# Optimization experiments

Hardware: AMD Instinct MI355X
Metric: run time of the kernel (lower is better)

## Reference

```python
import jax, jax.numpy as jnp
import numpy as np

# --- module hyperparameters (from init_kwargs / defaults) ---
CUTOFF = 4.5
NUM_RADIAL = 8
L_MAX = 2
RHO_U_DEGREE = 3
MAG_REF = 2.2
EPS = 1e-8
U_REF = max(MAG_REF * MAG_REF, EPS)

_centers_np = np.linspace(0.0, CUTOFF, NUM_RADIAL).astype(np.float32)
_spacing = float(_centers_np[1] - _centers_np[0]) if NUM_RADIAL > 1 else CUTOFF
BETA = 1.0 / max(_spacing * _spacing, EPS)
CENTERS = jnp.asarray(_centers_np)

N_ATOMS = 20000
N_NEIGH = 32


def cutoff_fn(r):
    x = jnp.clip(jnp.pi * r / CUTOFF, 0.0, jnp.pi)
    y = 0.5 * (jnp.cos(x) + 1.0)
    return y * (r < CUTOFF).astype(r.dtype)


def radial_basis(r):
    # r: [...], returns [..., NUM_RADIAL]
    diff = r[..., None] - CENTERS
    radial = jnp.exp(-BETA * diff * diff)
    return radial * cutoff_fn(r)[..., None]


def legendre_basis(x):
    # x: [...], returns [..., L_MAX + 1] via standard recurrence
    x = jnp.clip(x, -1.0, 1.0)
    polys = [jnp.ones_like(x)]
    if L_MAX >= 1:
        polys.append(x)
    for l in range(1, L_MAX):
        p_lp1 = ((2 * l + 1) * x * polys[-1] - l * polys[-2]) / (l + 1)
        polys.append(p_lp1)
    return jnp.stack(polys, axis=-1)


def setup_inputs() -> dict:
    key = jax.random.key(0)
    k1, k2, k3 = jax.random.split(key, 3)
    # positions in a small box so random-neighbor distances land inside the cutoff
    pos = jax.random.uniform(k1, (N_ATOMS, 3), dtype=jnp.float32) * 3.0
    mag = jax.random.normal(k2, (N_ATOMS, 3), dtype=jnp.float32)
    neigh_idx = jax.random.randint(k3, (N_ATOMS, N_NEIGH), 0, N_ATOMS)
    return {"pos": pos, "mag": mag, "neigh_idx": neigh_idx}


def reference(pos, mag, neigh_idx):
    N, K = neigh_idx.shape
    # gather neighbor geometry: [N, K, 3]
    vec = pos[neigh_idx] - pos[:, None, :]
    dist = jnp.sqrt(jnp.sum(vec * vec, axis=-1) + EPS)  # [N, K]
    f = radial_basis(dist)  # [N, K, R]

    # --- radial geometric channel ---
    rho_r = jnp.sum(f, axis=1)  # [N, R]

    # --- onsite longitudinal channel (power basis) ---
    u = jnp.sum(mag * mag, axis=-1)  # [N]
    u_norm = u / U_REF
    rho_u = jnp.stack([u_norm ** p for p in range(1, RHO_U_DEGREE + 1)], axis=-1)  # [N, 3]

    # --- neighbor magnetic channels ---
    mag_j = mag[neigh_idx]        # [N, K, 3]
    u_j = u_norm[neigh_idx]       # [N, K]
    rho_uj = jnp.einsum('nk,nkr->nr', u_j, f)                      # [N, R]
    s = jnp.einsum('nd,nkd->nk', mag, mag_j) / U_REF               # m_i . m_j / u_ref
    rho_s = jnp.einsum('nk,nkr->nr', s, f)                         # [N, R]

    # --- angular (triplet) channels, unique neighbor pairs j < k ---
    cos = jnp.einsum('njd,nkd->njk', vec, vec) / (dist[:, :, None] * dist[:, None, :] + EPS)
    P = legendre_basis(cos)  # [N, K, K, L+1]
    mask = jnp.triu(jnp.ones((K, K), dtype=f.dtype), k=1)  # j < k
    Pm = P * mask[None, :, :, None]

    A_rr = jnp.einsum('njkl,nja,nkb->nabl', Pm, f, f).reshape(N, -1)

    w_jk = jnp.einsum('njd,nkd->njk', mag_j, mag_j) / U_REF  # m_j . m_k / u_ref
    A_jk = jnp.einsum('njkl,nja,nkb->nabl', Pm * w_jk[..., None], f, f).reshape(N, -1)

    w_imm = s[:, :, None] * s[:, None, :]  # (m_i.m_j)(m_i.m_k) / u_ref^2
    A_imm = jnp.einsum('njkl,nja,nkb->nabl', Pm * w_imm[..., None], f, f).reshape(N, -1)

    # descriptor layout: rho_u | rho_r | A_rr | rho_uj | rho_s | A_jk | A_imm
    return jnp.concatenate([rho_u, rho_r, A_rr, rho_uj, rho_s, A_jk, A_imm], axis=-1)
```

## Files before the change

### kernel.cpp

```cpp
#include <hip/hip_runtime.h>

#define K 32
#define DESC 603

typedef _Float16 h8  __attribute__((ext_vector_type(8)));
typedef _Float16 h4v __attribute__((ext_vector_type(4)));
typedef __fp16   fp16x2 __attribute__((ext_vector_type(2)));
typedef float    f32x4 __attribute__((ext_vector_type(4)));

#define WAVE_LDS_FENCE()  __asm__ volatile("s_waitcnt lgkmcnt(0)" ::: "memory")
#define COMPILER_BARRIER() __asm__ volatile("" ::: "memory")

#define SFT   0
#define GTB   256
#define UHX   2304
#define UHY   2336
#define UHZ   2368
#define MJX   2400
#define MJY   2432
#define MJZ   2464
#define SSK   2496
#define SUK   2528
#define JPK   2560

__device__ __forceinline__ h8 h8splat(float x) {
    _Float16 h = (_Float16)x;
    h8 r = {h,h,h,h,h,h,h,h};
    return r;
}
__device__ __forceinline__ h8 bc(_Float16 h) {
    h8 r = {h,h,h,h,h,h,h,h};
    return r;
}
__device__ __forceinline__ h4v pk4(const f32x4& a) {
    fp16x2 lo = __builtin_amdgcn_cvt_pkrtz(a[0], a[1]);
    fp16x2 hi = __builtin_amdgcn_cvt_pkrtz(a[2], a[3]);
    h4v r;
    r[0] = (_Float16)lo[0]; r[1] = (_Float16)lo[1];
    r[2] = (_Float16)hi[0]; r[3] = (_Float16)hi[1];
    return r;
}

__global__ __launch_bounds__(256, 6)
void desc_kernel(const float* __restrict__ pos, const float* __restrict__ mag,
                 const int* __restrict__ nidx, float* __restrict__ out, int natoms)
{
    __shared__ __align__(16) _Float16 ldsbuf[4][2816];
    const int w = threadIdx.x >> 6;
    const int l = threadIdx.x & 63;
    int atom0 = blockIdx.x * 4 + w;
    const bool act = atom0 < natoms;
    if (!act) atom0 = natoms - 1;
    const int atom = __builtin_amdgcn_readfirstlane(atom0);
    _Float16* W = &ldsbuf[w][0];

    const int col  = l & 15;
    const int quad = l >> 4;
    const int k0   = quad * 8;

    const float CUTOFF  = 4.5f;
    const float SPACING = CUTOFF / 7.0f;
    const float BETA    = 1.0f / (SPACING * SPACING);
    const float INV_U   = 1.0f / 4.84f;
    const float INV_MAG = 1.0f / 2.2f;
    const float PI_F    = 3.14159265358979f;

    const float pix = pos[3*atom+0], piy = pos[3*atom+1], piz = pos[3*atom+2];
    const float mix = mag[3*atom+0], miy = mag[3*atom+1], miz = mag[3*atom+2];

    const int k = l & 31;
    const int n = nidx[atom*K + k];
    const float* src = (l < K) ? (pos + 3*n) : (mag + 3*n);
    const float v0 = src[0], v1 = src[1], v2 = src[2];

    if (l < K) {
        const float vx = v0 - pix, vy = v1 - piy, vz = v2 - piz;
        const float d  = sqrtf(vx*vx + vy*vy + vz*vz + 1e-8f);
        const float rd = 1.0f / d;
        const _Float16 hx = (_Float16)(vx*rd), hy = (_Float16)(vy*rd), hz = (_Float16)(vz*rd);
        W[UHX+k] = hx; W[UHY+k] = hy; W[UHZ+k] = hz;
        h4v jp = {hx, hy, hz, (_Float16)0.0f};
        *(h4v*)&W[JPK + k*8] = jp;
        float cut = 0.0f;
        if (d < CUTOFF) cut = 0.5f * (__cosf(PI_F * d / CUTOFF) + 1.0f);
        #pragma unroll
        for (int r = 0; r < 8; ++r) {
            const float diff = d - (float)r * SPACING;
            W[SFT + r*32 + k] = (_Float16)(__expf(-BETA * diff * diff) * cut);
        }
    } else {
        const float mx = v0*INV_MAG, my = v1*INV_MAG, mz = v2*INV_MAG;
        const float ss = (mix*v0 + miy*v1 + miz*v2) * INV_U;
        const float su = (v0*v0 + v1*v1 + v2*v2) * INV_U;
        const _Float16 hmx = (_Float16)mx, hmy = (_Float16)my, hmz = (_Float16)mz;
        const _Float16 hss = (_Float16)ss, hsu = (_Float16)su;
        W[MJX+k] = hmx; W[MJY+k] = hmy; W[MJZ+k] = hmz;
        W[SSK+k] = hss; W[SUK+k] = hsu;
        h4v jp = {hmx, hmy, hmz, hss};
        *(h4v*)&W[JPK + k*8 + 4] = jp;
    }
    if (l == 32 && act) {
        const float un = (mix*mix + miy*miy + miz*miz) * INV_U;
        out[atom*DESC+0] = un; out[atom*DESC+1] = un*un; out[atom*DESC+2] = un*un*un;
    }
    WAVE_LDS_FENCE();

    const h8 Bf   = *(const h8*)&W[SFT + (col&7)*32 + k0];
    const h8 uhx8 = *(const h8*)&W[UHX + k0];
    const h8 uhy8 = *(const h8*)&W[UHY + k0];
    const h8 uhz8 = *(const h8*)&W[UHZ + k0];
    const h8 mjx8 = *(const h8*)&W[MJX + k0];
    const h8 mjy8 = *(const h8*)&W[MJY + k0];
    const h8 mjz8 = *(const h8*)&W[MJZ + k0];
    const h8 ssk8 = *(const h8*)&W[SSK + k0];
    const h8 suk8 = *(const h8*)&W[SUK + k0];
    COMPILER_BARRIER();

    {
        h8 Ar = h8splat(0.0f);
        if      (col == 0) Ar = h8splat(1.0f);
        else if (col == 1) Ar = suk8;
        else if (col == 2) Ar = ssk8;
        f32x4 d = __builtin_amdgcn_mfma_f32_16x16x32_f16(Ar, Bf, (f32x4){0,0,0,0}, 0,0,0);
        if (act && quad == 0 && col < 8) {
            out[atom*DESC + 3   + col] = d[0];
            out[atom*DESC + 203 + col] = d[1];
            out[atom*DESC + 211 + col] = d[2];
        }
    }

    #pragma unroll
    for (int t = 0; t < 2; ++t) {
        const int j  = t*16 + col;
        const h8 jp  = *(const h8*)&W[JPK + j*8];
        h8 c = uhx8*bc(jp[0]) + uhy8*bc(jp[1]) + uhz8*bc(jp[2]);
        c = __builtin_elementwise_min(h8splat(1.0f),
            __builtin_elementwise_max(h8splat(-1.0f), c));
        const h8 P1 = c;
        const h8 P2 = c * c * h8splat(1.5f) - h8splat(0.5f);
        h8 wv  = mjx8*bc(jp[4]) + mjy8*bc(jp[5]) + mjz8*bc(jp[6]);
        h8 wiv = ssk8*bc(jp[7]);
        h8 mk;
        #pragma unroll
        for (int e = 0; e < 8; ++e)
            mk[e] = (_Float16)((k0 + e > j) ? 1.0f : 0.0f);

        const int tcol = t*16 + quad*4;
        const f32x4 z4 = {0,0,0,0};
        #pragma unroll
        for (int ch = 0; ch < 3; ++ch) {
            const h8 Bv = (ch == 0) ? mk : (ch == 1) ? wv*mk : wiv*mk;
            f32x4 a0 = __builtin_amdgcn_mfma_f32_16x16x32_f16(Bv,    Bf, z4, 0,0,0);
            f32x4 a1 = __builtin_amdgcn_mfma_f32_16x16x32_f16(Bv*P1, Bf, z4, 0,0,0);
            f32x4 a2 = __builtin_amdgcn_mfma_f32_16x16x32_f16(Bv*P2, Bf, z4, 0,0,0);
            if (col < 8) {
                const int row = ch*24 + col*3;
                *(h4v*)&W[GTB + (row+0)*32 + tcol] = pk4(a0);
                *(h4v*)&W[GTB + (row+1)*32 + tcol] = pk4(a1);
                *(h4v*)&W[GTB + (row+2)*32 + tcol] = pk4(a2);
            }
        }
    }
    WAVE_LDS_FENCE();

    #pragma unroll
    for (int nt = 0; nt < 5; ++nt) {
        const int n = nt*16 + col;
        const h8 Bg = *(const h8*)&W[GTB + n*32 + k0];
        const f32x4 d = __builtin_amdgcn_mfma_f32_16x16x32_f16(Bf, Bg, (f32x4){0,0,0,0}, 0,0,0);
        if (act && quad < 2 && n < 72) {
            const int ch  = n / 24;
            const int off = n - ch*24;
            const int cb  = (ch == 0) ? 11 : ((ch == 1) ? 219 : 411);
            const int base = atom*DESC + cb + off + quad*96;
            #pragma unroll
            for (int reg = 0; reg < 4; ++reg)
                out[base + reg*24] = d[reg];
        }
    }
}

extern "C" void kernel_launch(void* const* d_in, const int* in_sizes, int n_in,
                              void* d_out, int out_size, void* d_ws, size_t ws_size,
                              hipStream_t stream) {
    const float* pos  = (const float*)d_in[0];
    const float* mag  = (const float*)d_in[1];
    const int*   nidx = (const int*)d_in[2];
    float* out = (float*)d_out;
    const int n_atoms = in_sizes[2] / K;
    const int blocks = (n_atoms + 3) / 4;
    desc_kernel<<<blocks, 256, 0, stream>>>(pos, mag, nidx, out, n_atoms);
}
```

Baseline: 90.25 us.

## Process two atoms per wave and overlap the geometry and Gram buffers in LDS

Each wave now handles two atoms instead of one, using 128-thread blocks that still cover four atoms, so the gather, MFMA and store phases of two independent atoms can interleave. The per-atom LDS scratch is shrunk by placing the Gram-tile buffer over the radial-basis and direction arrays, which are already held in registers by the time they are overwritten. The aim is more instruction-level parallelism and less LDS use per atom. The cost is higher register pressure and a lower launch-bounds occupancy hint.

```diff
diff --git a/kernel.cpp b/kernel.cpp
--- a/kernel.cpp
+++ b/kernel.cpp
@@ -11,17 +11,17 @@
 #define WAVE_LDS_FENCE()  __asm__ volatile("s_waitcnt lgkmcnt(0)" ::: "memory")
 #define COMPILER_BARRIER() __asm__ volatile("" ::: "memory")
 
+#define GTB   0
 #define SFT   0
-#define GTB   256
-#define UHX   2304
-#define UHY   2336
-#define UHZ   2368
-#define MJX   2400
-#define MJY   2432
-#define MJZ   2464
-#define SSK   2496
-#define SUK   2528
-#define JPK   2560
+#define UHX   2048
+#define UHY   2080
+#define UHZ   2112
+#define MJX   2144
+#define MJY   2176
+#define MJZ   2208
+#define SSK   2240
+#define SUK   2272
+#define JPK   2304
 
 __device__ __forceinline__ h8 h8splat(float x) {
     _Float16 h = (_Float16)x;
@@ -41,19 +41,13 @@
     return r;
 }
 
-__global__ __launch_bounds__(256, 6)
+__global__ __launch_bounds__(128, 4)
 void desc_kernel(const float* __restrict__ pos, const float* __restrict__ mag,
                  const int* __restrict__ nidx, float* __restrict__ out, int natoms)
 {
-    __shared__ __align__(16) _Float16 ldsbuf[4][2816];
+    __shared__ __align__(16) _Float16 ldsbuf[4][2560];
     const int w = threadIdx.x >> 6;
     const int l = threadIdx.x & 63;
-    int atom0 = blockIdx.x * 4 + w;
-    const bool act = atom0 < natoms;
-    if (!act) atom0 = natoms - 1;
-    const int atom = __builtin_amdgcn_readfirstlane(atom0);
-    _Float16* W = &ldsbuf[w][0];
-
     const int col  = l & 15;
     const int quad = l >> 4;
     const int k0   = quad * 8;
@@ -65,117 +59,150 @@
     const float INV_MAG = 1.0f / 2.2f;
     const float PI_F    = 3.14159265358979f;
 
-    const float pix = pos[3*atom+0], piy = pos[3*atom+1], piz = pos[3*atom+2];
-    const float mix = mag[3*atom+0], miy = mag[3*atom+1], miz = mag[3*atom+2];
-
-    const int k = l & 31;
-    const int n = nidx[atom*K + k];
-    const float* src = (l < K) ? (pos + 3*n) : (mag + 3*n);
-    const float v0 = src[0], v1 = src[1], v2 = src[2];
-
-    if (l < K) {
-        const float vx = v0 - pix, vy = v1 - piy, vz = v2 - piz;
-        const float d  = sqrtf(vx*vx + vy*vy + vz*vz + 1e-8f);
-        const float rd = 1.0f / d;
-        const _Float16 hx = (_Float16)(vx*rd), hy = (_Float16)(vy*rd), hz = (_Float16)(vz*rd);
-        W[UHX+k] = hx; W[UHY+k] = hy; W[UHZ+k] = hz;
-        h4v jp = {hx, hy, hz, (_Float16)0.0f};
-        *(h4v*)&W[JPK + k*8] = jp;
-        float cut = 0.0f;
-        if (d < CUTOFF) cut = 0.5f * (__cosf(PI_F * d / CUTOFF) + 1.0f);
+    int       atomv[2];
+    bool      actv[2];
+    _Float16* Wv[2];
+    h8        Bfv[2];
+
+    #pragma unroll
+    for (int u = 0; u < 2; ++u) {
+        int a0 = blockIdx.x * 4 + w * 2 + u;
+        actv[u] = a0 < natoms;
+        if (!actv[u]) a0 = natoms - 1;
+        atomv[u] = __builtin_amdgcn_readfirstlane(a0);
+        Wv[u] = &ldsbuf[w * 2 + u][0];
+    }
+
+    #pragma unroll
+    for (int u = 0; u < 2; ++u) {
+        const int atom = atomv[u];
+        _Float16* W = Wv[u];
+        const float pix = pos[3*atom+0], piy = pos[3*atom+1], piz = pos[3*atom+2];
+        const float mix = mag[3*atom+0], miy = mag[3*atom+1], miz = mag[3*atom+2];
+
+        const int k = l & 31;
+        const int n = nidx[atom*K + k];
+        const float* src = (l < K) ? (pos + 3*n) : (mag + 3*n);
+        const float v0 = src[0], v1 = src[1], v2 = src[2];
+
+        if (l < K) {
+            const float vx = v0 - pix, vy = v1 - piy, vz = v2 - piz;
+            const float d  = sqrtf(vx*vx + vy*vy + vz*vz + 1e-8f);
+            const float rd = 1.0f / d;
+            const _Float16 hx = (_Float16)(vx*rd), hy = (_Float16)(vy*rd), hz = (_Float16)(vz*rd);
+            W[UHX+k] = hx; W[UHY+k] = hy; W[UHZ+k] = hz;
+            h4v jp = {hx, hy, hz, (_Float16)0.0f};
+            *(h4v*)&W[JPK + k*8] = jp;
+            float cut = 0.0f;
+            if (d < CUTOFF) cut = 0.5f * (__cosf(PI_F * d / CUTOFF) + 1.0f);
+            #pragma unroll
+            for (int r = 0; r < 8; ++r) {
+                const float diff = d - (float)r * SPACING;
+                W[SFT + r*32 + k] = (_Float16)(__expf(-BETA * diff * diff) * cut);
+            }
+        } else {
+            const float mx = v0*INV_MAG, my = v1*INV_MAG, mz = v2*INV_MAG;
+            const float ss = (mix*v0 + miy*v1 + miz*v2) * INV_U;
+            const float su = (v0*v0 + v1*v1 + v2*v2) * INV_U;
+            const _Float16 hmx = (_Float16)mx, hmy = (_Float16)my, hmz = (_Float16)mz;
+            W[MJX+k] = hmx; W[MJY+k] = hmy; W[MJZ+k] = hmz;
+            W[SSK+k] = (_Float16)ss; W[SUK+k] = (_Float16)su;
+            h4v jp = {hmx, hmy, hmz, (_Float16)ss};
+            *(h4v*)&W[JPK + k*8 + 4] = jp;
+        }
+        if (l == 32 && actv[u]) {
+            const float un = (mix*mix + miy*miy + miz*miz) * INV_U;
+            out[atom*DESC+0] = un; out[atom*DESC+1] = un*un; out[atom*DESC+2] = un*un*un;
+        }
+    }
+    WAVE_LDS_FENCE();
+
+    #pragma unroll
+    for (int u = 0; u < 2; ++u) {
+        const int atom = atomv[u];
+        const bool act = actv[u];
+        _Float16* W = Wv[u];
+
+        const h8 Bf   = *(const h8*)&W[SFT + (col&7)*32 + k0];
+        const h8 uhx8 = *(const h8*)&W[UHX + k0];
+        const h8 uhy8 = *(const h8*)&W[UHY + k0];
+        const h8 uhz8 = *(const h8*)&W[UHZ + k0];
+        const h8 mjx8 = *(const h8*)&W[MJX + k0];
+        const h8 mjy8 = *(const h8*)&W[MJY + k0];
+        const h8 mjz8 = *(const h8*)&W[MJZ + k0];
+        const h8 ssk8 = *(const h8*)&W[SSK + k0];
+        const h8 suk8 = *(const h8*)&W[SUK + k0];
+        Bfv[u] = Bf;
+        COMPILER_BARRIER();
+
+        {
+            h8 Ar = h8splat(0.0f);
+            if      (col == 0) Ar = h8splat(1.0f);
+            else if (col == 1) Ar = suk8;
+            else if (col == 2) Ar = ssk8;
+            f32x4 d = __builtin_amdgcn_mfma_f32_16x16x32_f16(Ar, Bf, (f32x4){0,0,0,0}, 0,0,0);
+            if (act && quad == 0 && col < 8) {
+                out[atom*DESC + 3   + col] = d[0];
+                out[atom*DESC + 203 + col] = d[1];
+                out[atom*DESC + 211 + col] = d[2];
+            }
+        }
+
         #pragma unroll
-        for (int r = 0; r < 8; ++r) {
-            const float diff = d - (float)r * SPACING;
-            W[SFT + r*32 + k] = (_Float16)(__expf(-BETA * diff * diff) * cut);
-        }
-    } else {
-        const float mx = v0*INV_MAG, my = v1*INV_MAG, mz = v2*INV_MAG;
-        const float ss = (mix*v0 + miy*v1 + miz*v2) * INV_U;
-        const float su = (v0*v0 + v1*v1 + v2*v2) * INV_U;
-        const _Float16 hmx = (_Float16)mx, hmy = (_Float16)my, hmz = (_Float16)mz;
-        const _Float16 hss = (_Float16)ss, hsu = (_Float16)su;
-        W[MJX+k] = hmx; W[MJY+k] = hmy; W[MJZ+k] = hmz;
-        W[SSK+k] = hss; W[SUK+k] = hsu;
-        h4v jp = {hmx, hmy, hmz, hss};
-        *(h4v*)&W[JPK + k*8 + 4] = jp;
-    }
-    if (l == 32 && act) {
-        const float un = (mix*mix + miy*miy + miz*miz) * INV_U;
-        out[atom*DESC+0] = un; out[atom*DESC+1] = un*un; out[atom*DESC+2] = un*un*un;
+        for (int t = 0; t < 2; ++t) {
+            const int j  = t*16 + col;
+            const h8 jp  = *(const h8*)&W[JPK + j*8];
+            h8 c = uhx8*bc(jp[0]) + uhy8*bc(jp[1]) + uhz8*bc(jp[2]);
+            c = __builtin_elementwise_min(h8splat(1.0f),
+                __builtin_elementwise_max(h8splat(-1.0f), c));
+            const h8 P1 = c;
+            const h8 P2 = c * c * h8splat(1.5f) - h8splat(0.5f);
+            h8 wv  = mjx8*bc(jp[4]) + mjy8*bc(jp[5]) + mjz8*bc(jp[6]);
+            h8 wiv = ssk8*bc(jp[7]);
+            h8 mk;
+            #pragma unroll
+            for (int e = 0; e < 8; ++e)
+                mk[e] = (_Float16)((k0 + e > j) ? 1.0f : 0.0f);
+
+            const int tcol = t*16 + quad*4;
+            const f32x4 z4 = {0,0,0,0};
+            #pragma unroll
+            for (int ch = 0; ch < 3; ++ch) {
+                const h8 Bv = (ch == 0) ? mk : (ch == 1) ? wv*mk : wiv*mk;
+                f32x4 a0 = __builtin_amdgcn_mfma_f32_16x16x32_f16(Bv,    Bf, z4, 0,0,0);
+                f32x4 a1 = __builtin_amdgcn_mfma_f32_16x16x32_f16(Bv*P1, Bf, z4, 0,0,0);
+                f32x4 a2 = __builtin_amdgcn_mfma_f32_16x16x32_f16(Bv*P2, Bf, z4, 0,0,0);
+                if (col < 8) {
+                    const int row = ch*24 + col*3;
+                    *(h4v*)&W[GTB + (row+0)*32 + tcol] = pk4(a0);
+                    *(h4v*)&W[GTB + (row+1)*32 + tcol] = pk4(a1);
+                    *(h4v*)&W[GTB + (row+2)*32 + tcol] = pk4(a2);
+                }
+            }
+        }
     }
     WAVE_LDS_FENCE();
 
-    const h8 Bf   = *(const h8*)&W[SFT + (col&7)*32 + k0];
-    const h8 uhx8 = *(const h8*)&W[UHX + k0];
-    const h8 uhy8 = *(const h8*)&W[UHY + k0];
-    const h8 uhz8 = *(const h8*)&W[UHZ + k0];
-    const h8 mjx8 = *(const h8*)&W[MJX + k0];
-    const h8 mjy8 = *(const h8*)&W[MJY + k0];
-    const h8 mjz8 = *(const h8*)&W[MJZ + k0];
-    const h8 ssk8 = *(const h8*)&W[SSK + k0];
-    const h8 suk8 = *(const h8*)&W[SUK + k0];
-    COMPILER_BARRIER();
-
-    {
-        h8 Ar = h8splat(0.0f);
-        if      (col == 0) Ar = h8splat(1.0f);
-        else if (col == 1) Ar = suk8;
-        else if (col == 2) Ar = ssk8;
-        f32x4 d = __builtin_amdgcn_mfma_f32_16x16x32_f16(Ar, Bf, (f32x4){0,0,0,0}, 0,0,0);
-        if (act && quad == 0 && col < 8) {
-            out[atom*DESC + 3   + col] = d[0];
-            out[atom*DESC + 203 + col] = d[1];
-            out[atom*DESC + 211 + col] = d[2];
-        }
-    }
-
-    #pragma unroll
-    for (int t = 0; t < 2; ++t) {
-        const int j  = t*16 + col;
-        const h8 jp  = *(const h8*)&W[JPK + j*8];
-        h8 c = uhx8*bc(jp[0]) + uhy8*bc(jp[1]) + uhz8*bc(jp[2]);
-        c = __builtin_elementwise_min(h8splat(1.0f),
-            __builtin_elementwise_max(h8splat(-1.0f), c));
-        const h8 P1 = c;
-        const h8 P2 = c * c * h8splat(1.5f) - h8splat(0.5f);
-        h8 wv  = mjx8*bc(jp[4]) + mjy8*bc(jp[5]) + mjz8*bc(jp[6]);
-        h8 wiv = ssk8*bc(jp[7]);
-        h8 mk;
+    #pragma unroll
+    for (int u = 0; u < 2; ++u) {
+        const int atom = atomv[u];
+        const bool act = actv[u];
+        _Float16* W = Wv[u];
+        const h8 Bf = Bfv[u];
         #pragma unroll
-        for (int e = 0; e < 8; ++e)
-            mk[e] = (_Float16)((k0 + e > j) ? 1.0f : 0.0f);
-
-        const int tcol = t*16 + quad*4;
-        const f32x4 z4 = {0,0,0,0};
-        #pragma unroll
-        for (int ch = 0; ch < 3; ++ch) {
-            const h8 Bv = (ch == 0) ? mk : (ch == 1) ? wv*mk : wiv*mk;
-            f32x4 a0 = __builtin_amdgcn_mfma_f32_16x16x32_f16(Bv,    Bf, z4, 0,0,0);
-            f32x4 a1 = __builtin_amdgcn_mfma_f32_16x16x32_f16(Bv*P1, Bf, z4, 0,0,0);
-            f32x4 a2 = __builtin_amdgcn_mfma_f32_16x16x32_f16(Bv*P2, Bf, z4, 0,0,0);
-            if (col < 8) {
-                const int row = ch*24 + col*3;
-                *(h4v*)&W[GTB + (row+0)*32 + tcol] = pk4(a0);
-                *(h4v*)&W[GTB + (row+1)*32 + tcol] = pk4(a1);
-                *(h4v*)&W[GTB + (row+2)*32 + tcol] = pk4(a2);
-            }
-        }
-    }
-    WAVE_LDS_FENCE();
-
-    #pragma unroll
-    for (int nt = 0; nt < 5; ++nt) {
-        const int n = nt*16 + col;
-        const h8 Bg = *(const h8*)&W[GTB + n*32 + k0];
-        const f32x4 d = __builtin_amdgcn_mfma_f32_16x16x32_f16(Bf, Bg, (f32x4){0,0,0,0}, 0,0,0);
-        if (act && quad < 2 && n < 72) {
-            const int ch  = n / 24;
-            const int off = n - ch*24;
-            const int cb  = (ch == 0) ? 11 : ((ch == 1) ? 219 : 411);
-            const int base = atom*DESC + cb + off + quad*96;
-            #pragma unroll
-            for (int reg = 0; reg < 4; ++reg)
-                out[base + reg*24] = d[reg];
+        for (int nt = 0; nt < 5; ++nt) {
+            const int n = nt*16 + col;
+            const h8 Bg = *(const h8*)&W[GTB + n*32 + k0];
+            const f32x4 d = __builtin_amdgcn_mfma_f32_16x16x32_f16(Bf, Bg, (f32x4){0,0,0,0}, 0,0,0);
+            if (act && quad < 2 && n < 72) {
+                const int ch  = n / 24;
+                const int off = n - ch*24;
+                const int cb  = (ch == 0) ? 11 : ((ch == 1) ? 219 : 411);
+                const int base = atom*DESC + cb + off + quad*96;
+                #pragma unroll
+                for (int reg = 0; reg < 4; ++reg)
+                    out[base + reg*24] = d[reg];
+            }
         }
     }
 }
@@ -189,5 +216,5 @@
     float* out = (float*)d_out;
     const int n_atoms = in_sizes[2] / K;
     const int blocks = (n_atoms + 3) / 4;
-    desc_kernel<<<blocks, 256, 0, stream>>>(pos, mag, nidx, out, n_atoms);
-}
+    desc_kernel<<<blocks, 128, 0, stream>>>(pos, mag, nidx, out, n_atoms);
+}
```

Result: slower. 94.19 us (+4.4%).
